# Kernel optimization log

Hardware: AMD Instinct MI355X
Metric: run time of the kernel (lower is better)

The kernel has to match this reference:

```python
import jax, jax.numpy as jnp
import numpy as np
from jax import lax

B, A, C, M = 8, 100000, 80, 32
ALPHA, GAMMA = 0.25, 2.0


def _calc_iou(a, b):
    # a: [A,4] anchors, b: [M,4] gt boxes -> [A,M]
    area = (b[:, 2] - b[:, 0]) * (b[:, 3] - b[:, 1])
    iw = jnp.clip(jnp.minimum(a[:, None, 2], b[None, :, 2]) - jnp.maximum(a[:, None, 0], b[None, :, 0]), 0.0)
    ih = jnp.clip(jnp.minimum(a[:, None, 3], b[None, :, 3]) - jnp.maximum(a[:, None, 1], b[None, :, 1]), 0.0)
    inter = iw * ih
    ua = jnp.clip(((a[:, 2] - a[:, 0]) * (a[:, 3] - a[:, 1]))[:, None] + area[None, :] - inter, 1e-8)
    return inter / ua


def _per_image(cls_p, reg, ann, anchor):
    # cls_p: [A,C], reg: [A,4], ann: [M,9], anchor: [A,4]
    p = jnp.clip(cls_p, 1e-4, 1.0 - 1e-4)
    iou = _calc_iou(anchor, ann[:, :4])            # [A,M]
    iou_max = jnp.max(iou, axis=1)                 # [A]
    iou_arg = jnp.argmax(iou, axis=1)              # [A]
    assigned = ann[iou_arg]                        # [A,9]
    pos = iou_max >= 0.5
    num_pos = jnp.sum(pos)

    # targets: -1 = ignore, 0 = background, one-hot for positives
    t = jnp.where(iou_max[:, None] < 0.4, 0.0, -1.0)
    cls_idx = lax.stop_gradient(assigned[:, 4]).astype(jnp.int32)
    t = jnp.where(pos[:, None], jax.nn.one_hot(cls_idx, C, dtype=p.dtype), t)

    alpha_f = jnp.where(t == 1.0, ALPHA, 1.0 - ALPHA)
    fw = jnp.where(t == 1.0, 1.0 - p, p)
    bce = -(t * jnp.log(p) + (1.0 - t) * jnp.log(1.0 - p))
    cls_loss = jnp.where(t != -1.0, alpha_f * fw ** GAMMA * bce, 0.0)
    cls_l = jnp.sum(cls_loss) / jnp.maximum(num_pos.astype(p.dtype), 1.0)

    aw = anchor[:, 2] - anchor[:, 0]
    ah = anchor[:, 3] - anchor[:, 1]
    acx = anchor[:, 0] + 0.5 * aw
    acy = anchor[:, 1] + 0.5 * ah
    gw_raw = assigned[:, 2] - assigned[:, 0]
    gh_raw = assigned[:, 3] - assigned[:, 1]
    gcx = assigned[:, 0] + 0.5 * gw_raw
    gcy = assigned[:, 1] + 0.5 * gh_raw
    gw = jnp.clip(gw_raw, 1.0)
    gh = jnp.clip(gh_raw, 1.0)
    tgt = jnp.stack([(gcx - acx) / aw, (gcy - acy) / ah,
                     jnp.log(gw / aw), jnp.log(gh / ah)], axis=1)
    tgt = tgt / jnp.array([0.1, 0.1, 0.2, 0.2], dtype=p.dtype)
    diff = jnp.abs(tgt - reg)
    sl1 = jnp.where(diff <= 1.0 / 9.0, 0.5 * 9.0 * diff ** 2, diff - 0.5 / 9.0)
    denom = jnp.maximum(num_pos.astype(p.dtype) * 4.0, 1.0)
    reg_l = jnp.where(num_pos > 0,
                      jnp.sum(jnp.where(pos[:, None], sl1, 0.0)) / denom,
                      jnp.zeros((), p.dtype))
    return cls_l, reg_l


def setup_inputs() -> dict:
    key = jax.random.key(0)
    k = jax.random.split(key, 8)
    classifications = jax.random.uniform(k[0], (B, A, C), jnp.float32, 1e-3, 1.0 - 1e-3)
    regressions = 0.1 * jax.random.normal(k[1], (B, A, 4), jnp.float32)
    ax0 = jax.random.uniform(k[2], (A,), jnp.float32, 0.0, 900.0)
    ay0 = jax.random.uniform(k[3], (A,), jnp.float32, 0.0, 900.0)
    awh = jax.random.uniform(k[4], (A, 2), jnp.float32, 16.0, 128.0)
    anchors = jnp.stack([ax0, ay0, ax0 + awh[:, 0], ay0 + awh[:, 1]], axis=1)[None]
    b0 = jax.random.uniform(k[5], (B, M, 2), jnp.float32, 0.0, 800.0)
    bwh = jax.random.uniform(k[6], (B, M, 2), jnp.float32, 8.0, 200.0)
    labels = jax.random.randint(k[7], (B, M, 1), 0, C).astype(jnp.float32)
    extra = jnp.zeros((B, M, 4), jnp.float32)  # cols 5..8: instance id + geo filler
    annotations = jnp.concatenate([b0, b0 + bwh, labels, extra], axis=-1)  # [B,M,9]
    return dict(classifications=classifications, regressions=regressions,
                anchors=anchors, annotations=annotations)


def reference(classifications, regressions, anchors, annotations):
    anchor = anchors[0]
    cls_l, reg_l = jax.vmap(_per_image, in_axes=(0, 0, 0, None))(
        classifications, regressions, annotations, anchor)
    return jnp.stack([jnp.mean(cls_l), jnp.mean(reg_l)])
```

## Files before the change

### kernel.cpp

```cpp
#include <hip/hip_runtime.h>

#define A_N 100000
#define B_N 8
#define C_N 80
#define M_N 32

typedef float vfloat4 __attribute__((ext_vector_type(4)));


__device__ __forceinline__ float bg_s4(vfloat4 v) {
    float p0 = fminf(fmaxf(v.x, 1e-4f), 1.0f - 1e-4f);
    float p1 = fminf(fmaxf(v.y, 1e-4f), 1.0f - 1e-4f);
    float p2 = fminf(fmaxf(v.z, 1e-4f), 1.0f - 1e-4f);
    float p3 = fminf(fmaxf(v.w, 1e-4f), 1.0f - 1e-4f);
    float l0 = __logf(1.0f - p0);
    float l1 = __logf(1.0f - p1);
    float l2 = __logf(1.0f - p2);
    float l3 = __logf(1.0f - p3);
    return fmaf(p0 * p0, l0, fmaf(p1 * p1, l1, fmaf(p2 * p2, l2, p3 * p3 * l3)));
}

__global__ __launch_bounds__(256, 5) void focal_main(
    const vfloat4* __restrict__ cls4,
    const float*  __restrict__ clsf,
    const float4* __restrict__ reg4,
    const float4* __restrict__ anc4,
    const float*  __restrict__ ann,
    float* __restrict__ cls_sum, float* __restrict__ reg_sum, int* __restrict__ npos)
{
    __shared__ float annL[M_N][6];
    __shared__ float redA[4];
    __shared__ float redB[4];
    __shared__ int   redI[4];

    const int b    = blockIdx.y;
    const int a0   = blockIdx.x * 256;
    const int tid  = threadIdx.x;
    const int lane = tid & 63;
    const int wid  = tid >> 6;

    if (tid < M_N) {
        const float* ar = ann + ((size_t)b * M_N + tid) * 9;
        float x0 = ar[0], y0 = ar[1], x1 = ar[2], y1 = ar[3], lb = ar[4];
        annL[tid][0] = x0; annL[tid][1] = y0;
        annL[tid][2] = x1; annL[tid][3] = y1;
        annL[tid][4] = lb; annL[tid][5] = (x1 - x0) * (y1 - y0);
    }
    __syncthreads();

    const int aw0    = a0 + (wid << 6);
    const int a      = aw0 + lane;
    const bool valid = a < A_N;
    const int vA     = min(64, A_N - aw0);
    const bool full  = (vA >= 64);
    const vfloat4* wbase = cls4 + ((size_t)b * A_N + aw0) * 20;

    float4 an = anc4[valid ? a : (A_N - 1)];

    float aw = an.z - an.x, ah = an.w - an.y;
    float aArea = aw * ah;
    float best = -1.0f; int bidx = 0;
    #pragma unroll 8
    for (int m = 0; m < M_N; ++m) {
        float iw = fminf(an.z, annL[m][2]) - fmaxf(an.x, annL[m][0]);
        float ih = fminf(an.w, annL[m][3]) - fmaxf(an.y, annL[m][1]);
        iw = fmaxf(iw, 0.0f); ih = fmaxf(ih, 0.0f);
        float inter = iw * ih;
        float ua = fmaxf(aArea + annL[m][5] - inter, 1e-8f);
        float iou = inter / ua;
        if (iou > best) { best = iou; bidx = m; }
    }
    const bool pos = valid && (best >= 0.5f);
    const int  st  = valid ? (pos ? 2 : (best < 0.4f ? 0 : 1)) : 1;
    const float myscale = (st != 1) ? -0.75f : 0.0f;

    float regacc = 0.0f;
    float clsacc = 0.0f;
    const unsigned long long bal = __ballot(pos);
    if (bal) {
        if (pos) {
            float4 r = reg4[(size_t)b * A_N + a];
            float gx0 = annL[bidx][0], gy0 = annL[bidx][1];
            float gx1 = annL[bidx][2], gy1 = annL[bidx][3];
            float gwr = gx1 - gx0, ghr = gy1 - gy0;
            float gcx = gx0 + 0.5f * gwr, gcy = gy0 + 0.5f * ghr;
            float gw = fmaxf(gwr, 1.0f), gh = fmaxf(ghr, 1.0f);
            float acx = an.x + 0.5f * aw, acy = an.y + 0.5f * ah;
            float t0 = (gcx - acx) / aw * 10.0f;
            float t1 = (gcy - acy) / ah * 10.0f;
            float t2 = __logf(gw / aw) * 5.0f;
            float t3 = __logf(gh / ah) * 5.0f;
            float d0 = fabsf(t0 - r.x), d1 = fabsf(t1 - r.y);
            float d2 = fabsf(t2 - r.z), d3 = fabsf(t3 - r.w);
            const float th = 1.0f / 9.0f;
            const float hs = 0.5f / 9.0f;
            regacc  = (d0 <= th) ? 4.5f * d0 * d0 : d0 - hs;
            regacc += (d1 <= th) ? 4.5f * d1 * d1 : d1 - hs;
            regacc += (d2 <= th) ? 4.5f * d2 * d2 : d2 - hs;
            regacc += (d3 <= th) ? 4.5f * d3 * d3 : d3 - hs;

            int ci = (int)annL[bidx][4];
            float pc = clsf[((size_t)b * A_N + a) * C_N + ci];
            pc = fminf(fmaxf(pc, 1e-4f), 1.0f - 1e-4f);
            float qc = 1.0f - pc;
            clsacc = -0.25f * qc * qc * __logf(pc) + 0.75f * pc * pc * __logf(qc);
        }
    }

    if (full) {
        vfloat4 buf[8];
        #pragma unroll
        for (int u = 0; u < 8; ++u)
            buf[u] = __builtin_nontemporal_load(wbase + (u << 6) + lane);
        #pragma unroll
        for (int u = 0; u < 20; ++u) {
            vfloat4 v = buf[u & 7];
            if (u + 8 < 20)
                buf[u & 7] = __builtin_nontemporal_load(wbase + ((u + 8) << 6) + lane);
            float s = __shfl(myscale, ((u << 6) + lane) / 20, 64);
            clsacc = fmaf(s, bg_s4(v), clsacc);
        }
    } else if (vA > 0) {
        const int n4 = vA * 20;
        for (int i = lane; i < n4; i += 64) {
            float s = __shfl(myscale, i / 20, 64);
            clsacc = fmaf(s, bg_s4(__builtin_nontemporal_load(wbase + i)), clsacc);
        }
    }

    #pragma unroll
    for (int o = 32; o > 0; o >>= 1) {
        regacc += __shfl_down(regacc, o, 64);
        clsacc += __shfl_down(clsacc, o, 64);
    }
    if (lane == 0) { redA[wid] = regacc; redB[wid] = clsacc; redI[wid] = __popcll(bal); }
    __syncthreads();
    if (tid == 0) {
        float rs = redA[0] + redA[1] + redA[2] + redA[3];
        float cs = redB[0] + redB[1] + redB[2] + redB[3];
        int   np = redI[0] + redI[1] + redI[2] + redI[3];
        if (rs != 0.0f) atomicAdd(&reg_sum[b], rs);
        if (np)         atomicAdd(&npos[b], np);
        atomicAdd(&cls_sum[b], cs);
    }
}

__global__ void focal_finalize(const float* __restrict__ cls_sum,
                               const float* __restrict__ reg_sum,
                               const int* __restrict__ npos,
                               float* __restrict__ out)
{
    if (threadIdx.x == 0) {
        float c = 0.0f, r = 0.0f;
        for (int b = 0; b < B_N; ++b) {
            float np = (float)npos[b];
            c += cls_sum[b] / fmaxf(np, 1.0f);
            r += (npos[b] > 0) ? reg_sum[b] / (4.0f * np) : 0.0f;
        }
        out[0] = c / (float)B_N;
        out[1] = r / (float)B_N;
    }
}

extern "C" void kernel_launch(void* const* d_in, const int* in_sizes, int n_in,
                              void* d_out, int out_size, void* d_ws, size_t ws_size,
                              hipStream_t stream) {
    const float* cls = (const float*)d_in[0];
    const float* reg = (const float*)d_in[1];
    const float* anc = (const float*)d_in[2];
    const float* ann = (const float*)d_in[3];

    float* ws      = (float*)d_ws;
    float* cls_sum = ws;
    float* reg_sum = ws + 8;
    int*   npos    = (int*)(ws + 16);

    (void)hipMemsetAsync(d_ws, 0, 24 * sizeof(float), stream);

    dim3 grid((A_N + 255) / 256, B_N);
    focal_main<<<grid, 256, 0, stream>>>(
        (const vfloat4*)cls, cls, (const float4*)reg, (const float4*)anc, ann,
        cls_sum, reg_sum, npos);

    focal_finalize<<<1, 64, 0, stream>>>(cls_sum, reg_sum, npos, (float*)d_out);
}
```

Before: 383.4 us.

## Split anchor assignment and class-probability streaming into separate kernels via bitmask

Splits the fused kernel in two. The first computes IoU assignment for all 8 images per anchor, using the anchor loaded once, and handles the positive-anchor regression and class corrections. It also writes a per-image ballot bitmask of anchors that are not ignored. A second, purely streaming kernel then reads the 256 MB classification tensor in 2048-vec4 tiles, looks up each anchor's scale from the bitmask and accumulates the background focal term. This decouples the latency-heavy IoU loop from the bandwidth-bound stream, at the cost of an extra launch, small bitmask reads with a per-element divide by 20, and more atomics in the assign kernel.

```diff
diff --git a/kernel.cpp b/kernel.cpp
--- a/kernel.cpp
+++ b/kernel.cpp
@@ -4,6 +4,10 @@
 #define B_N 8
 #define C_N 80
 #define M_N 32
+
+#define F4_PER_IMG 2000000
+#define WORDS_PER_IMG 1563
+#define STREAM_TILE 2048
 
 typedef float vfloat4 __attribute__((ext_vector_type(4)));
 
@@ -20,129 +24,146 @@
     return fmaf(p0 * p0, l0, fmaf(p1 * p1, l1, fmaf(p2 * p2, l2, p3 * p3 * l3)));
 }
 
-__global__ __launch_bounds__(256, 5) void focal_main(
-    const vfloat4* __restrict__ cls4,
+__global__ __launch_bounds__(256) void focal_assign(
     const float*  __restrict__ clsf,
     const float4* __restrict__ reg4,
     const float4* __restrict__ anc4,
     const float*  __restrict__ ann,
-    float* __restrict__ cls_sum, float* __restrict__ reg_sum, int* __restrict__ npos)
+    float* __restrict__ cls_sum, float* __restrict__ reg_sum, int* __restrict__ npos,
+    unsigned long long* __restrict__ bits)
 {
-    __shared__ float annL[M_N][6];
-    __shared__ float redA[4];
-    __shared__ float redB[4];
-    __shared__ int   redI[4];
-
-    const int b    = blockIdx.y;
-    const int a0   = blockIdx.x * 256;
+    __shared__ float annL[B_N][M_N][6];
+
     const int tid  = threadIdx.x;
     const int lane = tid & 63;
     const int wid  = tid >> 6;
-
-    if (tid < M_N) {
-        const float* ar = ann + ((size_t)b * M_N + tid) * 9;
-        float x0 = ar[0], y0 = ar[1], x1 = ar[2], y1 = ar[3], lb = ar[4];
-        annL[tid][0] = x0; annL[tid][1] = y0;
-        annL[tid][2] = x1; annL[tid][3] = y1;
-        annL[tid][4] = lb; annL[tid][5] = (x1 - x0) * (y1 - y0);
+    const int a0   = blockIdx.x * 256;
+    const int a    = a0 + tid;
+    const bool valid = a < A_N;
+    const int aw0  = a0 + (wid << 6);
+
+    for (int i = tid; i < B_N * M_N * 5; i += 256) {
+        int bb = i / (M_N * 5); int rem = i - bb * (M_N * 5);
+        int m = rem / 5, c = rem % 5;
+        annL[bb][m][c] = ann[((size_t)bb * M_N + m) * 9 + c];
     }
     __syncthreads();
-
-    const int aw0    = a0 + (wid << 6);
-    const int a      = aw0 + lane;
-    const bool valid = a < A_N;
-    const int vA     = min(64, A_N - aw0);
-    const bool full  = (vA >= 64);
-    const vfloat4* wbase = cls4 + ((size_t)b * A_N + aw0) * 20;
+    if (tid < B_N * M_N) {
+        int bb = tid / M_N, m = tid - bb * M_N;
+        annL[bb][m][5] = (annL[bb][m][2] - annL[bb][m][0]) * (annL[bb][m][3] - annL[bb][m][1]);
+    }
+    __syncthreads();
 
     float4 an = anc4[valid ? a : (A_N - 1)];
-
-    float aw = an.z - an.x, ah = an.w - an.y;
-    float aArea = aw * ah;
-    float best = -1.0f; int bidx = 0;
-    #pragma unroll 8
-    for (int m = 0; m < M_N; ++m) {
-        float iw = fminf(an.z, annL[m][2]) - fmaxf(an.x, annL[m][0]);
-        float ih = fminf(an.w, annL[m][3]) - fmaxf(an.y, annL[m][1]);
-        iw = fmaxf(iw, 0.0f); ih = fmaxf(ih, 0.0f);
-        float inter = iw * ih;
-        float ua = fmaxf(aArea + annL[m][5] - inter, 1e-8f);
-        float iou = inter / ua;
-        if (iou > best) { best = iou; bidx = m; }
-    }
-    const bool pos = valid && (best >= 0.5f);
-    const int  st  = valid ? (pos ? 2 : (best < 0.4f ? 0 : 1)) : 1;
-    const float myscale = (st != 1) ? -0.75f : 0.0f;
-
-    float regacc = 0.0f;
-    float clsacc = 0.0f;
-    const unsigned long long bal = __ballot(pos);
-    if (bal) {
-        if (pos) {
-            float4 r = reg4[(size_t)b * A_N + a];
-            float gx0 = annL[bidx][0], gy0 = annL[bidx][1];
-            float gx1 = annL[bidx][2], gy1 = annL[bidx][3];
-            float gwr = gx1 - gx0, ghr = gy1 - gy0;
-            float gcx = gx0 + 0.5f * gwr, gcy = gy0 + 0.5f * ghr;
-            float gw = fmaxf(gwr, 1.0f), gh = fmaxf(ghr, 1.0f);
-            float acx = an.x + 0.5f * aw, acy = an.y + 0.5f * ah;
-            float t0 = (gcx - acx) / aw * 10.0f;
-            float t1 = (gcy - acy) / ah * 10.0f;
-            float t2 = __logf(gw / aw) * 5.0f;
-            float t3 = __logf(gh / ah) * 5.0f;
-            float d0 = fabsf(t0 - r.x), d1 = fabsf(t1 - r.y);
-            float d2 = fabsf(t2 - r.z), d3 = fabsf(t3 - r.w);
-            const float th = 1.0f / 9.0f;
-            const float hs = 0.5f / 9.0f;
-            regacc  = (d0 <= th) ? 4.5f * d0 * d0 : d0 - hs;
-            regacc += (d1 <= th) ? 4.5f * d1 * d1 : d1 - hs;
-            regacc += (d2 <= th) ? 4.5f * d2 * d2 : d2 - hs;
-            regacc += (d3 <= th) ? 4.5f * d3 * d3 : d3 - hs;
-
-            int ci = (int)annL[bidx][4];
-            float pc = clsf[((size_t)b * A_N + a) * C_N + ci];
-            pc = fminf(fmaxf(pc, 1e-4f), 1.0f - 1e-4f);
-            float qc = 1.0f - pc;
-            clsacc = -0.25f * qc * qc * __logf(pc) + 0.75f * pc * pc * __logf(qc);
-        }
-    }
-
-    if (full) {
-        vfloat4 buf[8];
+    const float aw = an.z - an.x, ah = an.w - an.y;
+    const float aArea = aw * ah;
+    const float acx = an.x + 0.5f * aw, acy = an.y + 0.5f * ah;
+
+    for (int b = 0; b < B_N; ++b) {
+        float best = -1.0f; int bidx = 0;
+        #pragma unroll 8
+        for (int m = 0; m < M_N; ++m) {
+            float iw = fminf(an.z, annL[b][m][2]) - fmaxf(an.x, annL[b][m][0]);
+            float ih = fminf(an.w, annL[b][m][3]) - fmaxf(an.y, annL[b][m][1]);
+            iw = fmaxf(iw, 0.0f); ih = fmaxf(ih, 0.0f);
+            float inter = iw * ih;
+            float ua = fmaxf(aArea + annL[b][m][5] - inter, 1e-8f);
+            float iou = inter / ua;
+            if (iou > best) { best = iou; bidx = m; }
+        }
+        const bool pos = valid && (best >= 0.5f);
+        const int  st  = valid ? (pos ? 2 : (best < 0.4f ? 0 : 1)) : 1;
+
+        unsigned long long mask = __ballot(st != 1);
+        if (lane == 0 && aw0 < A_N)
+            bits[b * WORDS_PER_IMG + (aw0 >> 6)] = mask;
+
+        unsigned long long bal = __ballot(pos);
+        if (bal) {
+            float regacc = 0.0f, corr = 0.0f;
+            if (pos) {
+                float4 r = reg4[(size_t)b * A_N + a];
+                float gx0 = annL[b][bidx][0], gy0 = annL[b][bidx][1];
+                float gx1 = annL[b][bidx][2], gy1 = annL[b][bidx][3];
+                float gwr = gx1 - gx0, ghr = gy1 - gy0;
+                float gcx = gx0 + 0.5f * gwr, gcy = gy0 + 0.5f * ghr;
+                float gw = fmaxf(gwr, 1.0f), gh = fmaxf(ghr, 1.0f);
+                float t0 = (gcx - acx) / aw * 10.0f;
+                float t1 = (gcy - acy) / ah * 10.0f;
+                float t2 = __logf(gw / aw) * 5.0f;
+                float t3 = __logf(gh / ah) * 5.0f;
+                float d0 = fabsf(t0 - r.x), d1 = fabsf(t1 - r.y);
+                float d2 = fabsf(t2 - r.z), d3 = fabsf(t3 - r.w);
+                const float th = 1.0f / 9.0f;
+                const float hs = 0.5f / 9.0f;
+                regacc  = (d0 <= th) ? 4.5f * d0 * d0 : d0 - hs;
+                regacc += (d1 <= th) ? 4.5f * d1 * d1 : d1 - hs;
+                regacc += (d2 <= th) ? 4.5f * d2 * d2 : d2 - hs;
+                regacc += (d3 <= th) ? 4.5f * d3 * d3 : d3 - hs;
+
+                int ci = (int)annL[b][bidx][4];
+                float pc = clsf[((size_t)b * A_N + a) * C_N + ci];
+                pc = fminf(fmaxf(pc, 1e-4f), 1.0f - 1e-4f);
+                float qc = 1.0f - pc;
+                corr = -0.25f * qc * qc * __logf(pc) + 0.75f * pc * pc * __logf(qc);
+            }
+            #pragma unroll
+            for (int o = 32; o > 0; o >>= 1) {
+                regacc += __shfl_down(regacc, o, 64);
+                corr   += __shfl_down(corr, o, 64);
+            }
+            if (lane == 0) {
+                atomicAdd(&reg_sum[b], regacc);
+                atomicAdd(&cls_sum[b], corr);
+                atomicAdd(&npos[b], __popcll(bal));
+            }
+        }
+    }
+}
+
+__global__ __launch_bounds__(256) void focal_stream(
+    const vfloat4* __restrict__ cls4,
+    const unsigned long long* __restrict__ bits,
+    float* __restrict__ cls_sum)
+{
+    const int b   = blockIdx.y;
+    const int tid = threadIdx.x;
+    const int f0  = blockIdx.x * STREAM_TILE;
+    const vfloat4* base = cls4 + (size_t)b * F4_PER_IMG + f0;
+    const unsigned long long* wb = bits + b * WORDS_PER_IMG;
+
+    float acc = 0.0f;
+    if (f0 + STREAM_TILE <= F4_PER_IMG) {
         #pragma unroll
-        for (int u = 0; u < 8; ++u)
-            buf[u] = __builtin_nontemporal_load(wbase + (u << 6) + lane);
-        #pragma unroll
-        for (int u = 0; u < 20; ++u) {
-            vfloat4 v = buf[u & 7];
-            if (u + 8 < 20)
-                buf[u & 7] = __builtin_nontemporal_load(wbase + ((u + 8) << 6) + lane);
-            float s = __shfl(myscale, ((u << 6) + lane) / 20, 64);
-            clsacc = fmaf(s, bg_s4(v), clsacc);
-        }
-    } else if (vA > 0) {
-        const int n4 = vA * 20;
-        for (int i = lane; i < n4; i += 64) {
-            float s = __shfl(myscale, i / 20, 64);
-            clsacc = fmaf(s, bg_s4(__builtin_nontemporal_load(wbase + i)), clsacc);
+        for (int h = 0; h < 2; ++h) {
+            vfloat4 v[4]; float s[4];
+            #pragma unroll
+            for (int k = 0; k < 4; ++k) {
+                const int f  = ((h << 2) + k) * 256 + tid;
+                v[k] = __builtin_nontemporal_load(base + f);
+                const int ga = (f0 + f) / 20;
+                s[k] = ((wb[ga >> 6] >> (ga & 63)) & 1ULL) ? -0.75f : 0.0f;
+            }
+            #pragma unroll
+            for (int k = 0; k < 4; ++k)
+                acc = fmaf(s[k], bg_s4(v[k]), acc);
+        }
+    } else {
+        for (int f = tid; f0 + f < F4_PER_IMG; f += 256) {
+            vfloat4 v = __builtin_nontemporal_load(base + f);
+            const int ga = (f0 + f) / 20;
+            float s = ((wb[ga >> 6] >> (ga & 63)) & 1ULL) ? -0.75f : 0.0f;
+            acc = fmaf(s, bg_s4(v), acc);
         }
     }
 
     #pragma unroll
-    for (int o = 32; o > 0; o >>= 1) {
-        regacc += __shfl_down(regacc, o, 64);
-        clsacc += __shfl_down(clsacc, o, 64);
-    }
-    if (lane == 0) { redA[wid] = regacc; redB[wid] = clsacc; redI[wid] = __popcll(bal); }
+    for (int o = 32; o > 0; o >>= 1) acc += __shfl_down(acc, o, 64);
+    __shared__ float red[4];
+    if ((tid & 63) == 0) red[tid >> 6] = acc;
     __syncthreads();
-    if (tid == 0) {
-        float rs = redA[0] + redA[1] + redA[2] + redA[3];
-        float cs = redB[0] + redB[1] + redB[2] + redB[3];
-        int   np = redI[0] + redI[1] + redI[2] + redI[3];
-        if (rs != 0.0f) atomicAdd(&reg_sum[b], rs);
-        if (np)         atomicAdd(&npos[b], np);
-        atomicAdd(&cls_sum[b], cs);
-    }
+    if (tid == 0)
+        atomicAdd(&cls_sum[b], red[0] + red[1] + red[2] + red[3]);
 }
 
 __global__ void focal_finalize(const float* __restrict__ cls_sum,
@@ -174,13 +195,18 @@
     float* cls_sum = ws;
     float* reg_sum = ws + 8;
     int*   npos    = (int*)(ws + 16);
-
-    (void)hipMemsetAsync(d_ws, 0, 24 * sizeof(float), stream);
-
-    dim3 grid((A_N + 255) / 256, B_N);
-    focal_main<<<grid, 256, 0, stream>>>(
-        (const vfloat4*)cls, cls, (const float4*)reg, (const float4*)anc, ann,
-        cls_sum, reg_sum, npos);
+    unsigned long long* bits = (unsigned long long*)((char*)d_ws + 128);
+
+    (void)hipMemsetAsync(d_ws, 0, 128, stream);
+
+    dim3 gridA((A_N + 255) / 256, 1);
+    focal_assign<<<gridA, 256, 0, stream>>>(
+        cls, (const float4*)reg, (const float4*)anc, ann,
+        cls_sum, reg_sum, npos, bits);
+
+    dim3 gridS((F4_PER_IMG + STREAM_TILE - 1) / STREAM_TILE, B_N);
+    focal_stream<<<gridS, 256, 0, stream>>>(
+        (const vfloat4*)cls, bits, cls_sum);
 
     focal_finalize<<<1, 64, 0, stream>>>(cls_sum, reg_sum, npos, (float*)d_out);
 }
```

Measured after the change: 541.6 us. 41.3% more time.
